# Kernel tuning notes

Measured on AMD Instinct MI355X. Metric: run time of the kernel, lower is better.

## Reference

```python
import jax, jax.numpy as jnp
import numpy as np

B = 16384       # batch of peptide samples
M = 15          # max_peptide_size
R = 64          # aa_rep_size
P = 34          # number of pocket positions
F = 9           # filter_size
A = 20          # alphabet size


def setup_inputs() -> dict:
    key = jax.random.key(0)
    k1, k2, k3, k4 = jax.random.split(key, 4)
    peptide_encoding = jax.random.normal(k1, (B, M, R), dtype=jnp.float32)
    pocket_aa_idx = jax.random.randint(k2, (B, P), 0, A, dtype=jnp.int32)
    adj_mask = jax.random.randint(k3, (B, P, M), 0, 2, dtype=jnp.int32)
    # one trainable 1-D filter of length F per alphabet letter ('uniform' init)
    kernels = jax.random.uniform(k4, (A, F), dtype=jnp.float32, minval=-0.05, maxval=0.05)
    return {"peptide_encoding": peptide_encoding, "pocket_aa_idx": pocket_aa_idx,
            "adj_mask": adj_mask, "kernels": kernels}


def reference(peptide_encoding, pocket_aa_idx, adj_mask, kernels):
    # Per pocket position p of sample b: filter = kernels[pocket_aa_idx[b,p]]  [B,P,F]
    filt = kernels[pocket_aa_idx]
    # Convolution is linear, so sum the adjacent peptide-position encodings first:
    # s[b,p,r] = sum_m adj_mask[b,p,m] * peptide_encoding[b,m,r]   -> [B,P,R]
    s = jnp.einsum('bpm,bmr->bpr', adj_mask.astype(peptide_encoding.dtype), peptide_encoding)
    # Full convolution along the representation axis: output length R + F - 1
    conv1 = jax.vmap(jax.vmap(lambda a, b: jnp.convolve(a, b, mode='full')))
    out = conv1(s, filt)  # [B, P, R+F-1]
    return out
```

## Files before the change

kernel.cpp:

```cpp
#include <hip/hip_runtime.h>

#define MM 15
#define RR 64
#define PP 34
#define FF 9
#define AA 20
#define OW 72
#define SP 84
#define KS 12
#define AJ 16

__global__ __launch_bounds__(256)
void ppc_kernel(const float* __restrict__ pe,
                const int*   __restrict__ idx,
                const int*   __restrict__ adj,
                const float* __restrict__ kernels,
                float*       __restrict__ out)
{
    const int b = blockIdx.x;
    const int t = threadIdx.x;

    __shared__ float s_pe[MM * RR];
    __shared__ float s_kern[AA * KS];
    __shared__ float s_adjf[PP * AJ];
    __shared__ int   s_idx[PP];
    __shared__ float s_s[PP * SP];

    const float* peb  = pe  + (size_t)b * (MM * RR);
    const int*   adjb = adj + (size_t)b * (PP * MM);

    if (t < (MM * RR) / 4)
        *(float4*)&s_pe[t * 4] = *(const float4*)&peb[t * 4];
    if (t < AA * FF) {
        int a = (unsigned)t / FF, j = t - a * FF;
        s_kern[a * KS + j] = kernels[t];
    }
    for (int i = t; i < PP * MM; i += 256) {
        int p = (unsigned)i / MM, m = i - p * MM;
        s_adjf[p * AJ + m] = (float)adjb[i];
    }
    if (t < PP) s_idx[t] = idx[(size_t)b * PP + t];
    if (t < PP * 5) {
        int p = (unsigned)t / 5, k = t - p * 5;
        int off = p * SP + (k < 2 ? k * 4 : 72 + (k - 2) * 4);
        *(float4*)&s_s[off] = make_float4(0.f, 0.f, 0.f, 0.f);
    }
    __syncthreads();

    {
        const int w = t >> 6;
        const int r = t & 63;
        float pv[MM];
        #pragma unroll
        for (int m = 0; m < MM; ++m) pv[m] = s_pe[m * RR + r];
        #pragma unroll
        for (int j = 0; j < 9; ++j) {
            const int p = w + 4 * j;
            if (p < PP) {
                const float* g = &s_adjf[p * AJ];
                const float4 g0 = *(const float4*)&g[0];
                const float4 g1 = *(const float4*)&g[4];
                const float4 g2 = *(const float4*)&g[8];
                const float4 g3 = *(const float4*)&g[12];
                float acc;
                acc  = g0.x * pv[0]  + g0.y * pv[1]  + g0.z * pv[2]  + g0.w * pv[3];
                acc += g1.x * pv[4]  + g1.y * pv[5]  + g1.z * pv[6]  + g1.w * pv[7];
                acc += g2.x * pv[8]  + g2.y * pv[9]  + g2.z * pv[10] + g2.w * pv[11];
                acc += g3.x * pv[12] + g3.y * pv[13] + g3.z * pv[14];
                s_s[p * SP + 8 + r] = acc;
            }
        }
    }
    __syncthreads();

    float* outb = out + (size_t)b * (PP * OW);
    const int c  = t & 15;
    const int q  = t >> 4;
    const int r0 = c << 2;

    auto do_p = [&](const int p) {
        float kf[FF];
        {
            const float* kb = &s_kern[s_idx[p] * KS];
            const float4 k0 = *(const float4*)&kb[0];
            const float4 k1 = *(const float4*)&kb[4];
            kf[0]=k0.x; kf[1]=k0.y; kf[2]=k0.z; kf[3]=k0.w;
            kf[4]=k1.x; kf[5]=k1.y; kf[6]=k1.z; kf[7]=k1.w;
            kf[8]=kb[8];
        }
        const float* row = &s_s[p * SP];
        {
            float w[12];
            *(float4*)&w[0] = *(const float4*)&row[r0];
            *(float4*)&w[4] = *(const float4*)&row[r0 + 4];
            *(float4*)&w[8] = *(const float4*)&row[r0 + 8];
            float ax=0, ay=0, az=0, aw=0;
            #pragma unroll
            for (int j = 0; j < FF; ++j) {
                const float k = kf[j];
                ax += k * w[8  - j];
                ay += k * w[9  - j];
                az += k * w[10 - j];
                aw += k * w[11 - j];
            }
            *(float4*)&outb[p * OW + r0] = make_float4(ax, ay, az, aw);
        }
        if (c < 2) {
            const int o0 = 64 + r0;
            float w[12];
            *(float4*)&w[0] = *(const float4*)&row[o0];
            *(float4*)&w[4] = *(const float4*)&row[o0 + 4];
            *(float4*)&w[8] = *(const float4*)&row[o0 + 8];
            float ax=0, ay=0, az=0, aw=0;
            #pragma unroll
            for (int j = 0; j < FF; ++j) {
                const float k = kf[j];
                ax += k * w[8  - j];
                ay += k * w[9  - j];
                az += k * w[10 - j];
                aw += k * w[11 - j];
            }
            *(float4*)&outb[p * OW + o0] = make_float4(ax, ay, az, aw);
        }
    };

    do_p(q);
    do_p(q + 16);
    if (q + 32 < PP) do_p(q + 32);
}

extern "C" void kernel_launch(void* const* d_in, const int* in_sizes, int n_in,
                              void* d_out, int out_size, void* d_ws, size_t ws_size,
                              hipStream_t stream) {
    const float* pe      = (const float*)d_in[0];
    const int*   idx     = (const int*)  d_in[1];
    const int*   adj     = (const int*)  d_in[2];
    const float* kernels = (const float*)d_in[3];
    float*       out     = (float*)d_out;

    const int B = in_sizes[0] / (MM * RR);
    ppc_kernel<<<B, 256, 0, stream>>>(pe, idx, adj, kernels, out);
}
```

Baseline: 76.74 us.

## Give each wavefront its own rows, dropping the block barrier and pe LDS staging

```diff
diff --git a/kernel.cpp b/kernel.cpp
--- a/kernel.cpp
+++ b/kernel.cpp
@@ -20,7 +20,6 @@
     const int b = blockIdx.x;
     const int t = threadIdx.x;
 
-    __shared__ float s_pe[MM * RR];
     __shared__ float s_kern[AA * KS];
     __shared__ float s_adjf[PP * AJ];
     __shared__ int   s_idx[PP];
@@ -29,8 +28,13 @@
     const float* peb  = pe  + (size_t)b * (MM * RR);
     const int*   adjb = adj + (size_t)b * (PP * MM);
 
-    if (t < (MM * RR) / 4)
-        *(float4*)&s_pe[t * 4] = *(const float4*)&peb[t * 4];
+    const int w    = t >> 6;
+    const int lane = t & 63;
+
+    float pv[MM];
+    #pragma unroll
+    for (int m = 0; m < MM; ++m) pv[m] = peb[m * RR + lane];
+
     if (t < AA * FF) {
         int a = (unsigned)t / FF, j = t - a * FF;
         s_kern[a * KS + j] = kernels[t];
@@ -47,86 +51,61 @@
     }
     __syncthreads();
 
-    {
-        const int w = t >> 6;
-        const int r = t & 63;
-        float pv[MM];
-        #pragma unroll
-        for (int m = 0; m < MM; ++m) pv[m] = s_pe[m * RR + r];
-        #pragma unroll
-        for (int j = 0; j < 9; ++j) {
-            const int p = w + 4 * j;
-            if (p < PP) {
-                const float* g = &s_adjf[p * AJ];
-                const float4 g0 = *(const float4*)&g[0];
-                const float4 g1 = *(const float4*)&g[4];
-                const float4 g2 = *(const float4*)&g[8];
-                const float4 g3 = *(const float4*)&g[12];
-                float acc;
-                acc  = g0.x * pv[0]  + g0.y * pv[1]  + g0.z * pv[2]  + g0.w * pv[3];
-                acc += g1.x * pv[4]  + g1.y * pv[5]  + g1.z * pv[6]  + g1.w * pv[7];
-                acc += g2.x * pv[8]  + g2.y * pv[9]  + g2.z * pv[10] + g2.w * pv[11];
-                acc += g3.x * pv[12] + g3.y * pv[13] + g3.z * pv[14];
-                s_s[p * SP + 8 + r] = acc;
-            }
+    #pragma unroll
+    for (int j = 0; j < 9; ++j) {
+        const int p = w + 4 * j;
+        if (p < PP) {
+            const float* g = &s_adjf[p * AJ];
+            const float4 g0 = *(const float4*)&g[0];
+            const float4 g1 = *(const float4*)&g[4];
+            const float4 g2 = *(const float4*)&g[8];
+            const float4 g3 = *(const float4*)&g[12];
+            float acc;
+            acc  = g0.x * pv[0]  + g0.y * pv[1]  + g0.z * pv[2]  + g0.w * pv[3];
+            acc += g1.x * pv[4]  + g1.y * pv[5]  + g1.z * pv[6]  + g1.w * pv[7];
+            acc += g2.x * pv[8]  + g2.y * pv[9]  + g2.z * pv[10] + g2.w * pv[11];
+            acc += g3.x * pv[12] + g3.y * pv[13] + g3.z * pv[14];
+            s_s[p * SP + 8 + lane] = acc;
         }
     }
-    __syncthreads();
 
     float* outb = out + (size_t)b * (PP * OW);
-    const int c  = t & 15;
-    const int q  = t >> 4;
-    const int r0 = c << 2;
 
-    auto do_p = [&](const int p) {
-        float kf[FF];
-        {
+    const int rowk = (unsigned)lane / 18u;
+    const int q18  = lane - 18 * rowk;
+    const int o0   = q18 << 2;
+
+    #pragma unroll
+    for (int k = 0; k < 3; ++k) {
+        const int j = 3 * k + rowk;
+        const int p = w + 4 * j;
+        if (rowk < 3 && p < PP) {
             const float* kb = &s_kern[s_idx[p] * KS];
             const float4 k0 = *(const float4*)&kb[0];
             const float4 k1 = *(const float4*)&kb[4];
+            float kf[FF];
             kf[0]=k0.x; kf[1]=k0.y; kf[2]=k0.z; kf[3]=k0.w;
             kf[4]=k1.x; kf[5]=k1.y; kf[6]=k1.z; kf[7]=k1.w;
             kf[8]=kb[8];
-        }
-        const float* row = &s_s[p * SP];
-        {
-            float w[12];
-            *(float4*)&w[0] = *(const float4*)&row[r0];
-            *(float4*)&w[4] = *(const float4*)&row[r0 + 4];
-            *(float4*)&w[8] = *(const float4*)&row[r0 + 8];
+
+            const float* row = &s_s[p * SP];
+            float wv[12];
+            *(float4*)&wv[0] = *(const float4*)&row[o0];
+            *(float4*)&wv[4] = *(const float4*)&row[o0 + 4];
+            *(float4*)&wv[8] = *(const float4*)&row[o0 + 8];
+
             float ax=0, ay=0, az=0, aw=0;
             #pragma unroll
-            for (int j = 0; j < FF; ++j) {
-                const float k = kf[j];
-                ax += k * w[8  - j];
-                ay += k * w[9  - j];
-                az += k * w[10 - j];
-                aw += k * w[11 - j];
-            }
-            *(float4*)&outb[p * OW + r0] = make_float4(ax, ay, az, aw);
-        }
-        if (c < 2) {
-            const int o0 = 64 + r0;
-            float w[12];
-            *(float4*)&w[0] = *(const float4*)&row[o0];
-            *(float4*)&w[4] = *(const float4*)&row[o0 + 4];
-            *(float4*)&w[8] = *(const float4*)&row[o0 + 8];
-            float ax=0, ay=0, az=0, aw=0;
-            #pragma unroll
-            for (int j = 0; j < FF; ++j) {
-                const float k = kf[j];
-                ax += k * w[8  - j];
-                ay += k * w[9  - j];
-                az += k * w[10 - j];
-                aw += k * w[11 - j];
+            for (int jj = 0; jj < FF; ++jj) {
+                const float kk = kf[jj];
+                ax += kk * wv[8  - jj];
+                ay += kk * wv[9  - jj];
+                az += kk * wv[10 - jj];
+                aw += kk * wv[11 - jj];
             }
             *(float4*)&outb[p * OW + o0] = make_float4(ax, ay, az, aw);
         }
-    };
-
-    do_p(q);
-    do_p(q + 16);
-    if (q + 32 < PP) do_p(q + 32);
+    }
 }
 
 extern "C" void kernel_launch(void* const* d_in, const int* in_sizes, int n_in,
```

Measured after the change: 73.72 us. 3.9% less time.
